# Optimization experiments

Hardware: AMD Instinct MI355X
Metric: run time of the kernel (lower is better)

Reference implementation:

```python
import jax, jax.numpy as jnp
import numpy as np

ALPHA = 1.0

def setup_inputs() -> dict:
    key = jax.random.key(0)
    k1, k2 = jax.random.split(key)
    N, D, K = 131072, 256, 256
    inputs = jax.random.normal(k1, (N, D), dtype=jnp.float32)
    clusters = jax.random.normal(k2, (K, D), dtype=jnp.float32)
    return {"inputs": inputs, "clusters": clusters}


def reference(inputs, clusters):
    x_sq = jnp.sum(inputs * inputs, axis=1, keepdims=True)          # (N,1)
    c_sq = jnp.sum(clusters * clusters, axis=1)[None, :]            # (1,K)
    cross = jnp.einsum('nd,kd->nk', inputs, clusters)               # (N,K)
    dist2 = jnp.maximum(x_sq + c_sq - 2.0 * cross, 0.0)
    q = 1.0 / (1.0 + dist2 / ALPHA)
    q = q ** ((ALPHA + 1.0) / 2.0)
    q = q / jnp.sum(q, axis=1, keepdims=True)
    return q
```

## Files before the change

kernel.cpp:

```cpp
#include <hip/hip_runtime.h>
#include <hip/hip_bf16.h>


#define DDIM 256
#define KCL 256
#define BM 128
#define DCHUNK 64

typedef __bf16 v8bf __attribute__((ext_vector_type(8)));
typedef float f32x4 __attribute__((ext_vector_type(4)));

__global__ __launch_bounds__(512, 4) void cluster_soft_assign(
    const float* __restrict__ X, const float* __restrict__ C,
    float* __restrict__ out)
{
    __shared__ __align__(16) __bf16 Bs[KCL * DCHUNK];
    __shared__ float csq_s[KCL];

    const int t    = threadIdx.x;
    const int wave = t >> 6;
    const int lane = t & 63;
    const int lr   = lane & 15;
    const int kg   = lane >> 4;

    const long brow = (long)blockIdx.x * BM;
    const int  rowl = wave * 16 + lr;
    const float* xrow = X + (brow + rowl) * DDIM;

    const int scol = t >> 1;
    const int sd0  = (t & 1) * 32;

    f32x4 acc[16];
#pragma unroll
    for (int i = 0; i < 16; ++i) { acc[i][0]=0.f; acc[i][1]=0.f; acc[i][2]=0.f; acc[i][3]=0.f; }

    float csq_part = 0.f;
    float xsq_part = 0.f;

    for (int c = 0; c < 4; ++c) {
        const int dbase = c * DCHUNK;

        const float4 a0 = *(const float4*)(xrow + dbase + kg * 8);
        const float4 a1 = *(const float4*)(xrow + dbase + kg * 8 + 4);
        const float4 a2 = *(const float4*)(xrow + dbase + 32 + kg * 8);
        const float4 a3 = *(const float4*)(xrow + dbase + 32 + kg * 8 + 4);

        if (c) __syncthreads();

        const float* cp = C + (size_t)scol * DDIM + dbase + sd0;
#pragma unroll
        for (int g = 0; g < 4; ++g) {
            const float4 f0 = *(const float4*)(cp + g * 8);
            const float4 f1 = *(const float4*)(cp + g * 8 + 4);
            csq_part += f0.x*f0.x + f0.y*f0.y + f0.z*f0.z + f0.w*f0.w
                      + f1.x*f1.x + f1.y*f1.y + f1.z*f1.z + f1.w*f1.w;
            v8bf pk;
            pk[0]=(__bf16)f0.x; pk[1]=(__bf16)f0.y; pk[2]=(__bf16)f0.z; pk[3]=(__bf16)f0.w;
            pk[4]=(__bf16)f1.x; pk[5]=(__bf16)f1.y; pk[6]=(__bf16)f1.z; pk[7]=(__bf16)f1.w;
            const int dl = sd0 + g * 8;
            *(v8bf*)&Bs[scol * DCHUNK + (dl ^ ((scol & 7) << 3))] = pk;
        }
        __syncthreads();

        xsq_part += a0.x*a0.x + a0.y*a0.y + a0.z*a0.z + a0.w*a0.w
                  + a1.x*a1.x + a1.y*a1.y + a1.z*a1.z + a1.w*a1.w
                  + a2.x*a2.x + a2.y*a2.y + a2.z*a2.z + a2.w*a2.w
                  + a3.x*a3.x + a3.y*a3.y + a3.z*a3.z + a3.w*a3.w;

        v8bf af0, af1;
        af0[0]=(__bf16)a0.x; af0[1]=(__bf16)a0.y; af0[2]=(__bf16)a0.z; af0[3]=(__bf16)a0.w;
        af0[4]=(__bf16)a1.x; af0[5]=(__bf16)a1.y; af0[6]=(__bf16)a1.z; af0[7]=(__bf16)a1.w;
        af1[0]=(__bf16)a2.x; af1[1]=(__bf16)a2.y; af1[2]=(__bf16)a2.z; af1[3]=(__bf16)a2.w;
        af1[4]=(__bf16)a3.x; af1[5]=(__bf16)a3.y; af1[6]=(__bf16)a3.z; af1[7]=(__bf16)a3.w;

        const int dl0 = kg * 8;
        const int dl1 = 32 + kg * 8;
#pragma unroll
        for (int tl = 0; tl < 16; ++tl) {
            const int col = tl * 16 + lr;
            const v8bf bf0 = *(const v8bf*)&Bs[col * DCHUNK + (dl0 ^ ((col & 7) << 3))];
            acc[tl] = __builtin_amdgcn_mfma_f32_16x16x32_bf16(af0, bf0, acc[tl], 0, 0, 0);
        }
#pragma unroll
        for (int tl = 0; tl < 16; ++tl) {
            const int col = tl * 16 + lr;
            const v8bf bf1 = *(const v8bf*)&Bs[col * DCHUNK + (dl1 ^ ((col & 7) << 3))];
            acc[tl] = __builtin_amdgcn_mfma_f32_16x16x32_bf16(af1, bf1, acc[tl], 0, 0, 0);
        }
    }

    csq_part += __shfl_xor(csq_part, 1);
    if ((t & 1) == 0) csq_s[scol] = csq_part;

    float xsq = xsq_part;
    xsq += __shfl_xor(xsq, 16);
    xsq += __shfl_xor(xsq, 32);

    __syncthreads();

#pragma unroll
    for (int j = 0; j < 4; ++j) {
        const long orow = brow + wave * 16 + kg * 4 + j;
        const float xs = __shfl(xsq, kg * 4 + j);
        float qv[16];
        float s = 0.f;
#pragma unroll
        for (int tl = 0; tl < 16; ++tl) {
            const float cs = csq_s[tl * 16 + lr];
            float d2 = xs + cs - 2.f * acc[tl][j];
            d2 = fmaxf(d2, 0.f);
            const float q = 1.f / (1.f + d2);
            qv[tl] = q;
            s += q;
        }
        s += __shfl_xor(s, 1);
        s += __shfl_xor(s, 2);
        s += __shfl_xor(s, 4);
        s += __shfl_xor(s, 8);
        const float r = 1.f / s;
        float* op = out + orow * DDIM + lr;
#pragma unroll
        for (int tl = 0; tl < 16; ++tl) op[tl * 16] = qv[tl] * r;
    }
}

extern "C" void kernel_launch(void* const* d_in, const int* in_sizes, int n_in,
                              void* d_out, int out_size, void* d_ws, size_t ws_size,
                              hipStream_t stream) {
    const float* X = (const float*)d_in[0];
    const float* C = (const float*)d_in[1];
    float* out = (float*)d_out;
    const int N = in_sizes[0] / DDIM;
    const int nblocks = N / BM;
    hipLaunchKernelGGL(cluster_soft_assign, dim3(nblocks), dim3(512), 0, stream,
                       X, C, out);
}
```

Baseline: 277.8 us.

## Make blocks persistent with full cluster matrix resident in LDS

Converts the kernel to a persistent design: 256 blocks of 1024 threads each convert and store the whole 256x256 bf16 cluster matrix in LDS once, then loop over several 256-row tiles. This removes the per-block reconversion of C and the per-chunk barriers, and adds a one-step register prefetch of X rows in the MFMA loop. The trade-off is 128KB of LDS per block, which allows only one block per CU. With 16 waves per block and a serial MFMA/epilogue per iteration, latency hiding may suffer, and the iters computation assumes N divides evenly.

```diff
diff --git a/kernel.cpp b/kernel.cpp
--- a/kernel.cpp
+++ b/kernel.cpp
@@ -4,17 +4,16 @@
 
 #define DDIM 256
 #define KCL 256
-#define BM 128
-#define DCHUNK 64
 
 typedef __bf16 v8bf __attribute__((ext_vector_type(8)));
 typedef float f32x4 __attribute__((ext_vector_type(4)));
 
-__global__ __launch_bounds__(512, 4) void cluster_soft_assign(
+__global__ __launch_bounds__(1024, 4) void cluster_soft_assign(
     const float* __restrict__ X, const float* __restrict__ C,
-    float* __restrict__ out)
+    float* __restrict__ out, int iters)
 {
-    __shared__ __align__(16) __bf16 Bs[KCL * DCHUNK];
+    __shared__ __align__(16) __bf16 Bs[KCL * DDIM];
+    __shared__ float red[1024];
     __shared__ float csq_s[KCL];
 
     const int t    = threadIdx.x;
@@ -23,33 +22,14 @@
     const int lr   = lane & 15;
     const int kg   = lane >> 4;
 
-    const long brow = (long)blockIdx.x * BM;
-    const int  rowl = wave * 16 + lr;
-    const float* xrow = X + (brow + rowl) * DDIM;
-
-    const int scol = t >> 1;
-    const int sd0  = (t & 1) * 32;
-
-    f32x4 acc[16];
+    {
+        const int col = t & 255;
+        const int dq  = (t >> 8) * 64;
+        const int sw  = (col & 7) << 3;
+        const float* cp = C + (size_t)col * DDIM + dq;
+        float csq_part = 0.f;
 #pragma unroll
-    for (int i = 0; i < 16; ++i) { acc[i][0]=0.f; acc[i][1]=0.f; acc[i][2]=0.f; acc[i][3]=0.f; }
-
-    float csq_part = 0.f;
-    float xsq_part = 0.f;
-
-    for (int c = 0; c < 4; ++c) {
-        const int dbase = c * DCHUNK;
-
-        const float4 a0 = *(const float4*)(xrow + dbase + kg * 8);
-        const float4 a1 = *(const float4*)(xrow + dbase + kg * 8 + 4);
-        const float4 a2 = *(const float4*)(xrow + dbase + 32 + kg * 8);
-        const float4 a3 = *(const float4*)(xrow + dbase + 32 + kg * 8 + 4);
-
-        if (c) __syncthreads();
-
-        const float* cp = C + (size_t)scol * DDIM + dbase + sd0;
-#pragma unroll
-        for (int g = 0; g < 4; ++g) {
+        for (int g = 0; g < 8; ++g) {
             const float4 f0 = *(const float4*)(cp + g * 8);
             const float4 f1 = *(const float4*)(cp + g * 8 + 4);
             csq_part += f0.x*f0.x + f0.y*f0.y + f0.z*f0.z + f0.w*f0.w
@@ -57,70 +37,78 @@
             v8bf pk;
             pk[0]=(__bf16)f0.x; pk[1]=(__bf16)f0.y; pk[2]=(__bf16)f0.z; pk[3]=(__bf16)f0.w;
             pk[4]=(__bf16)f1.x; pk[5]=(__bf16)f1.y; pk[6]=(__bf16)f1.z; pk[7]=(__bf16)f1.w;
-            const int dl = sd0 + g * 8;
-            *(v8bf*)&Bs[scol * DCHUNK + (dl ^ ((scol & 7) << 3))] = pk;
+            const int d = dq + g * 8;
+            *(v8bf*)&Bs[col * DDIM + (d ^ sw)] = pk;
         }
-        __syncthreads();
-
-        xsq_part += a0.x*a0.x + a0.y*a0.y + a0.z*a0.z + a0.w*a0.w
-                  + a1.x*a1.x + a1.y*a1.y + a1.z*a1.z + a1.w*a1.w
-                  + a2.x*a2.x + a2.y*a2.y + a2.z*a2.z + a2.w*a2.w
-                  + a3.x*a3.x + a3.y*a3.y + a3.z*a3.z + a3.w*a3.w;
-
-        v8bf af0, af1;
-        af0[0]=(__bf16)a0.x; af0[1]=(__bf16)a0.y; af0[2]=(__bf16)a0.z; af0[3]=(__bf16)a0.w;
-        af0[4]=(__bf16)a1.x; af0[5]=(__bf16)a1.y; af0[6]=(__bf16)a1.z; af0[7]=(__bf16)a1.w;
-        af1[0]=(__bf16)a2.x; af1[1]=(__bf16)a2.y; af1[2]=(__bf16)a2.z; af1[3]=(__bf16)a2.w;
-        af1[4]=(__bf16)a3.x; af1[5]=(__bf16)a3.y; af1[6]=(__bf16)a3.z; af1[7]=(__bf16)a3.w;
-
-        const int dl0 = kg * 8;
-        const int dl1 = 32 + kg * 8;
-#pragma unroll
-        for (int tl = 0; tl < 16; ++tl) {
-            const int col = tl * 16 + lr;
-            const v8bf bf0 = *(const v8bf*)&Bs[col * DCHUNK + (dl0 ^ ((col & 7) << 3))];
-            acc[tl] = __builtin_amdgcn_mfma_f32_16x16x32_bf16(af0, bf0, acc[tl], 0, 0, 0);
-        }
-#pragma unroll
-        for (int tl = 0; tl < 16; ++tl) {
-            const int col = tl * 16 + lr;
-            const v8bf bf1 = *(const v8bf*)&Bs[col * DCHUNK + (dl1 ^ ((col & 7) << 3))];
-            acc[tl] = __builtin_amdgcn_mfma_f32_16x16x32_bf16(af1, bf1, acc[tl], 0, 0, 0);
-        }
+        red[t] = csq_part;
     }
-
-    csq_part += __shfl_xor(csq_part, 1);
-    if ((t & 1) == 0) csq_s[scol] = csq_part;
-
-    float xsq = xsq_part;
-    xsq += __shfl_xor(xsq, 16);
-    xsq += __shfl_xor(xsq, 32);
-
+    __syncthreads();
+    if (t < 256) csq_s[t] = red[t] + red[t + 256] + red[t + 512] + red[t + 768];
     __syncthreads();
 
+    const int swl = (lr & 7) << 3;
+
+    for (int it = 0; it < iters; ++it) {
+        const size_t rowbase = ((size_t)blockIdx.x * iters + it) * 256;
+        const float* xrow = X + (rowbase + wave * 16 + lr) * DDIM + kg * 8;
+
+        f32x4 acc[16];
 #pragma unroll
-    for (int j = 0; j < 4; ++j) {
-        const long orow = brow + wave * 16 + kg * 4 + j;
-        const float xs = __shfl(xsq, kg * 4 + j);
-        float qv[16];
-        float s = 0.f;
+        for (int i = 0; i < 16; ++i) { acc[i][0]=0.f; acc[i][1]=0.f; acc[i][2]=0.f; acc[i][3]=0.f; }
+        float xsq = 0.f;
+
+        float4 c0 = *(const float4*)(xrow + 0);
+        float4 c1 = *(const float4*)(xrow + 4);
 #pragma unroll
-        for (int tl = 0; tl < 16; ++tl) {
-            const float cs = csq_s[tl * 16 + lr];
-            float d2 = xs + cs - 2.f * acc[tl][j];
-            d2 = fmaxf(d2, 0.f);
-            const float q = 1.f / (1.f + d2);
-            qv[tl] = q;
-            s += q;
+        for (int kc = 0; kc < 8; ++kc) {
+            float4 n0, n1;
+            if (kc < 7) {
+                n0 = *(const float4*)(xrow + (kc + 1) * 32);
+                n1 = *(const float4*)(xrow + (kc + 1) * 32 + 4);
+            }
+            xsq += c0.x*c0.x + c0.y*c0.y + c0.z*c0.z + c0.w*c0.w
+                 + c1.x*c1.x + c1.y*c1.y + c1.z*c1.z + c1.w*c1.w;
+            v8bf af;
+            af[0]=(__bf16)c0.x; af[1]=(__bf16)c0.y; af[2]=(__bf16)c0.z; af[3]=(__bf16)c0.w;
+            af[4]=(__bf16)c1.x; af[5]=(__bf16)c1.y; af[6]=(__bf16)c1.z; af[7]=(__bf16)c1.w;
+
+            const int dbase = kc * 32 + kg * 8;
+#pragma unroll
+            for (int tl = 0; tl < 16; ++tl) {
+                const int col = tl * 16 + lr;
+                const v8bf bf = *(const v8bf*)&Bs[col * DDIM + (dbase ^ swl)];
+                acc[tl] = __builtin_amdgcn_mfma_f32_16x16x32_bf16(af, bf, acc[tl], 0, 0, 0);
+            }
+            c0 = n0; c1 = n1;
         }
-        s += __shfl_xor(s, 1);
-        s += __shfl_xor(s, 2);
-        s += __shfl_xor(s, 4);
-        s += __shfl_xor(s, 8);
-        const float r = 1.f / s;
-        float* op = out + orow * DDIM + lr;
+
+        xsq += __shfl_xor(xsq, 16);
+        xsq += __shfl_xor(xsq, 32);
+
 #pragma unroll
-        for (int tl = 0; tl < 16; ++tl) op[tl * 16] = qv[tl] * r;
+        for (int j = 0; j < 4; ++j) {
+            const size_t orow = rowbase + wave * 16 + kg * 4 + j;
+            const float xs = __shfl(xsq, kg * 4 + j);
+            float qv[16];
+            float s = 0.f;
+#pragma unroll
+            for (int tl = 0; tl < 16; ++tl) {
+                const float cs = csq_s[tl * 16 + lr];
+                float d2 = xs + cs - 2.f * acc[tl][j];
+                d2 = fmaxf(d2, 0.f);
+                const float q = 1.f / (1.f + d2);
+                qv[tl] = q;
+                s += q;
+            }
+            s += __shfl_xor(s, 1);
+            s += __shfl_xor(s, 2);
+            s += __shfl_xor(s, 4);
+            s += __shfl_xor(s, 8);
+            const float r = 1.f / s;
+            float* op = out + orow * DDIM + lr;
+#pragma unroll
+            for (int tl = 0; tl < 16; ++tl) op[tl * 16] = qv[tl] * r;
+        }
     }
 }
 
@@ -131,7 +119,9 @@
     const float* C = (const float*)d_in[1];
     float* out = (float*)d_out;
     const int N = in_sizes[0] / DDIM;
-    const int nblocks = N / BM;
-    hipLaunchKernelGGL(cluster_soft_assign, dim3(nblocks), dim3(512), 0, stream,
-                       X, C, out);
+    int nblocks = N / 256;
+    if (nblocks > 256) nblocks = 256;
+    const int iters = N / (nblocks * 256);
+    hipLaunchKernelGGL(cluster_soft_assign, dim3(nblocks), dim3(1024), 0, stream,
+                       X, C, out, iters);
 }
```

Result: slower. 600.0 us (+116.0%).

## Double-buffer cluster tiles, prefetch X rows, and stage output through LDS for vector stores

Applied to the files above, without the earlier changes.

The cluster chunk tiles in LDS are now double-buffered, and the next chunk's global load overlaps the MFMA work on the current chunk. All X row data is loaded up front. In the epilogue, c_sq values are hoisted into registers and the divisions use hardware rcp. Output goes through an LDS transpose so each row is written with float4 coalesced stores. The costs are higher register and LDS use, a lower occupancy hint (2 instead of 4), and the reduced precision of rcp.

```diff
diff --git a/kernel.cpp b/kernel.cpp
--- a/kernel.cpp
+++ b/kernel.cpp
@@ -10,11 +10,11 @@
 typedef __bf16 v8bf __attribute__((ext_vector_type(8)));
 typedef float f32x4 __attribute__((ext_vector_type(4)));
 
-__global__ __launch_bounds__(512, 4) void cluster_soft_assign(
+__global__ __launch_bounds__(512, 2) void cluster_soft_assign(
     const float* __restrict__ X, const float* __restrict__ C,
     float* __restrict__ out)
 {
-    __shared__ __align__(16) __bf16 Bs[KCL * DCHUNK];
+    __shared__ __align__(16) __bf16 Bs[2][KCL * DCHUNK];
     __shared__ float csq_s[KCL];
 
     const int t    = threadIdx.x;
@@ -23,93 +23,117 @@
     const int lr   = lane & 15;
     const int kg   = lane >> 4;
 
-    const long brow = (long)blockIdx.x * BM;
-    const int  rowl = wave * 16 + lr;
-    const float* xrow = X + (brow + rowl) * DDIM;
+    const size_t brow = (size_t)blockIdx.x * BM;
+    const float* xrow = X + (brow + wave * 16 + lr) * DDIM + kg * 8;
 
     const int scol = t >> 1;
     const int sd0  = (t & 1) * 32;
+    const float* cbase = C + (size_t)scol * DDIM + sd0;
 
-    f32x4 acc[16];
-#pragma unroll
-    for (int i = 0; i < 16; ++i) { acc[i][0]=0.f; acc[i][1]=0.f; acc[i][2]=0.f; acc[i][3]=0.f; }
+    float4 sr[8];
+    float  csq_part = 0.f;
 
-    float csq_part = 0.f;
-    float xsq_part = 0.f;
-
-    for (int c = 0; c < 4; ++c) {
-        const int dbase = c * DCHUNK;
-
-        const float4 a0 = *(const float4*)(xrow + dbase + kg * 8);
-        const float4 a1 = *(const float4*)(xrow + dbase + kg * 8 + 4);
-        const float4 a2 = *(const float4*)(xrow + dbase + 32 + kg * 8);
-        const float4 a3 = *(const float4*)(xrow + dbase + 32 + kg * 8 + 4);
-
-        if (c) __syncthreads();
-
-        const float* cp = C + (size_t)scol * DDIM + dbase + sd0;
+    auto stage_load = [&](int c) {
+        const float* cp = cbase + c * DCHUNK;
 #pragma unroll
         for (int g = 0; g < 4; ++g) {
-            const float4 f0 = *(const float4*)(cp + g * 8);
-            const float4 f1 = *(const float4*)(cp + g * 8 + 4);
+            sr[2*g]   = *(const float4*)(cp + g * 8);
+            sr[2*g+1] = *(const float4*)(cp + g * 8 + 4);
+        }
+    };
+    auto stage_write = [&](int b) {
+#pragma unroll
+        for (int g = 0; g < 4; ++g) {
+            const float4 f0 = sr[2*g], f1 = sr[2*g+1];
             csq_part += f0.x*f0.x + f0.y*f0.y + f0.z*f0.z + f0.w*f0.w
                       + f1.x*f1.x + f1.y*f1.y + f1.z*f1.z + f1.w*f1.w;
             v8bf pk;
             pk[0]=(__bf16)f0.x; pk[1]=(__bf16)f0.y; pk[2]=(__bf16)f0.z; pk[3]=(__bf16)f0.w;
             pk[4]=(__bf16)f1.x; pk[5]=(__bf16)f1.y; pk[6]=(__bf16)f1.z; pk[7]=(__bf16)f1.w;
             const int dl = sd0 + g * 8;
-            *(v8bf*)&Bs[scol * DCHUNK + (dl ^ ((scol & 7) << 3))] = pk;
+            *(v8bf*)&Bs[b][scol * DCHUNK + (dl ^ ((scol & 7) << 3))] = pk;
         }
-        __syncthreads();
+    };
 
-        xsq_part += a0.x*a0.x + a0.y*a0.y + a0.z*a0.z + a0.w*a0.w
-                  + a1.x*a1.x + a1.y*a1.y + a1.z*a1.z + a1.w*a1.w
-                  + a2.x*a2.x + a2.y*a2.y + a2.z*a2.z + a2.w*a2.w
-                  + a3.x*a3.x + a3.y*a3.y + a3.z*a3.z + a3.w*a3.w;
+    float4 ax[16];
+#pragma unroll
+    for (int c = 0; c < 4; ++c) {
+        ax[4*c+0] = *(const float4*)(xrow + c*64);
+        ax[4*c+1] = *(const float4*)(xrow + c*64 + 4);
+        ax[4*c+2] = *(const float4*)(xrow + c*64 + 32);
+        ax[4*c+3] = *(const float4*)(xrow + c*64 + 36);
+    }
+    stage_load(0);
 
-        v8bf af0, af1;
-        af0[0]=(__bf16)a0.x; af0[1]=(__bf16)a0.y; af0[2]=(__bf16)a0.z; af0[3]=(__bf16)a0.w;
-        af0[4]=(__bf16)a1.x; af0[5]=(__bf16)a1.y; af0[6]=(__bf16)a1.z; af0[7]=(__bf16)a1.w;
-        af1[0]=(__bf16)a2.x; af1[1]=(__bf16)a2.y; af1[2]=(__bf16)a2.z; af1[3]=(__bf16)a2.w;
-        af1[4]=(__bf16)a3.x; af1[5]=(__bf16)a3.y; af1[6]=(__bf16)a3.z; af1[7]=(__bf16)a3.w;
+    float xsq = 0.f;
+    v8bf af[8];
+#pragma unroll
+    for (int c = 0; c < 4; ++c) {
+        const float4 a0 = ax[4*c], a1 = ax[4*c+1], a2 = ax[4*c+2], a3 = ax[4*c+3];
+        xsq += a0.x*a0.x + a0.y*a0.y + a0.z*a0.z + a0.w*a0.w
+             + a1.x*a1.x + a1.y*a1.y + a1.z*a1.z + a1.w*a1.w
+             + a2.x*a2.x + a2.y*a2.y + a2.z*a2.z + a2.w*a2.w
+             + a3.x*a3.x + a3.y*a3.y + a3.z*a3.z + a3.w*a3.w;
+        v8bf f0, f1;
+        f0[0]=(__bf16)a0.x; f0[1]=(__bf16)a0.y; f0[2]=(__bf16)a0.z; f0[3]=(__bf16)a0.w;
+        f0[4]=(__bf16)a1.x; f0[5]=(__bf16)a1.y; f0[6]=(__bf16)a1.z; f0[7]=(__bf16)a1.w;
+        f1[0]=(__bf16)a2.x; f1[1]=(__bf16)a2.y; f1[2]=(__bf16)a2.z; f1[3]=(__bf16)a2.w;
+        f1[4]=(__bf16)a3.x; f1[5]=(__bf16)a3.y; f1[6]=(__bf16)a3.z; f1[7]=(__bf16)a3.w;
+        af[2*c] = f0; af[2*c+1] = f1;
+    }
+    xsq += __shfl_xor(xsq, 16);
+    xsq += __shfl_xor(xsq, 32);
 
-        const int dl0 = kg * 8;
-        const int dl1 = 32 + kg * 8;
+    stage_write(0);
+    stage_load(1);
+    __syncthreads();
+
+    f32x4 acc[16];
+#pragma unroll
+    for (int i = 0; i < 16; ++i) { acc[i][0]=0.f; acc[i][1]=0.f; acc[i][2]=0.f; acc[i][3]=0.f; }
+
+#pragma unroll
+    for (int c = 0; c < 4; ++c) {
+        const int b = c & 1;
 #pragma unroll
         for (int tl = 0; tl < 16; ++tl) {
             const int col = tl * 16 + lr;
-            const v8bf bf0 = *(const v8bf*)&Bs[col * DCHUNK + (dl0 ^ ((col & 7) << 3))];
-            acc[tl] = __builtin_amdgcn_mfma_f32_16x16x32_bf16(af0, bf0, acc[tl], 0, 0, 0);
+            const v8bf bf = *(const v8bf*)&Bs[b][col * DCHUNK + ((kg*8) ^ ((col & 7) << 3))];
+            acc[tl] = __builtin_amdgcn_mfma_f32_16x16x32_bf16(af[2*c], bf, acc[tl], 0, 0, 0);
         }
 #pragma unroll
         for (int tl = 0; tl < 16; ++tl) {
             const int col = tl * 16 + lr;
-            const v8bf bf1 = *(const v8bf*)&Bs[col * DCHUNK + (dl1 ^ ((col & 7) << 3))];
-            acc[tl] = __builtin_amdgcn_mfma_f32_16x16x32_bf16(af1, bf1, acc[tl], 0, 0, 0);
+            const v8bf bf = *(const v8bf*)&Bs[b][col * DCHUNK + ((32 + kg*8) ^ ((col & 7) << 3))];
+            acc[tl] = __builtin_amdgcn_mfma_f32_16x16x32_bf16(af[2*c+1], bf, acc[tl], 0, 0, 0);
+        }
+        if (c < 3) {
+            __syncthreads();
+            stage_write(b ^ 1);
+            if (c < 2) stage_load(c + 2);
+            __syncthreads();
         }
     }
 
     csq_part += __shfl_xor(csq_part, 1);
     if ((t & 1) == 0) csq_s[scol] = csq_part;
-
-    float xsq = xsq_part;
-    xsq += __shfl_xor(xsq, 16);
-    xsq += __shfl_xor(xsq, 32);
-
     __syncthreads();
 
+    float cs[16];
+#pragma unroll
+    for (int tl = 0; tl < 16; ++tl) cs[tl] = csq_s[tl * 16 + lr];
+
+    float* tb = (float*)&Bs[0][0];
+    const int twbase = wave * 1024;
 #pragma unroll
     for (int j = 0; j < 4; ++j) {
-        const long orow = brow + wave * 16 + kg * 4 + j;
         const float xs = __shfl(xsq, kg * 4 + j);
         float qv[16];
         float s = 0.f;
 #pragma unroll
         for (int tl = 0; tl < 16; ++tl) {
-            const float cs = csq_s[tl * 16 + lr];
-            float d2 = xs + cs - 2.f * acc[tl][j];
-            d2 = fmaxf(d2, 0.f);
-            const float q = 1.f / (1.f + d2);
+            const float d2 = fmaxf(xs + cs[tl] - 2.f * acc[tl][j], 0.f);
+            const float q = __builtin_amdgcn_rcpf(1.f + d2);
             qv[tl] = q;
             s += q;
         }
@@ -117,10 +141,18 @@
         s += __shfl_xor(s, 2);
         s += __shfl_xor(s, 4);
         s += __shfl_xor(s, 8);
-        const float r = 1.f / s;
-        float* op = out + orow * DDIM + lr;
+        const float r = __builtin_amdgcn_rcpf(s);
 #pragma unroll
-        for (int tl = 0; tl < 16; ++tl) op[tl * 16] = qv[tl] * r;
+        for (int tl = 0; tl < 16; ++tl) {
+            const int col = tl * 16 + lr;
+            tb[twbase + kg * 256 + (col ^ (kg * 8))] = qv[tl] * r;
+        }
+        asm volatile("s_waitcnt lgkmcnt(0)" ::: "memory");
+#pragma unroll
+        for (int i = 0; i < 4; ++i) {
+            const f32x4 rv = *(const f32x4*)&tb[twbase + i * 256 + ((lane * 4) ^ (i * 8))];
+            *(f32x4*)&out[(brow + wave * 16 + i * 4 + j) * DDIM + lane * 4] = rv;
+        }
     }
 }
 
```

Result: faster. 271.9 us (-2.1%).

## Precompute bf16 swizzled clusters once and stream them into LDS with global_load_lds

Applied to the files above, without the earlier changes.

A small prep kernel converts the cluster matrix to bf16 in the swizzled LDS layout and computes the cluster squared norms once into workspace. The main kernel then copies each 64-wide chunk straight into LDS with global_load_lds instead of every block reloading fp32 clusters, converting them and re-reducing the norms. The main kernel also halves the rows per block with 256 threads and prefetches the next X chunk before the MFMAs. It uses hardware rcp approximations and stages each output row through LDS so stores are full-row coalesced float4 writes. The trade-offs are an extra launch and slightly less precise reciprocals.

```diff
diff --git a/kernel.cpp b/kernel.cpp
--- a/kernel.cpp
+++ b/kernel.cpp
@@ -3,16 +3,42 @@
 
 
 #define DDIM 256
-#define KCL 256
-#define BM 128
+#define KCL  256
+#define BM   64
 #define DCHUNK 64
 
 typedef __bf16 v8bf __attribute__((ext_vector_type(8)));
+typedef __bf16 v4bf __attribute__((ext_vector_type(4)));
 typedef float f32x4 __attribute__((ext_vector_type(4)));
 
-__global__ __launch_bounds__(512, 4) void cluster_soft_assign(
-    const float* __restrict__ X, const float* __restrict__ C,
-    float* __restrict__ out)
+__global__ __launch_bounds__(256) void prep_clusters(
+    const float* __restrict__ C, __bf16* __restrict__ wsB, float* __restrict__ wsCsq)
+{
+    const int t = threadIdx.x;
+    const int wave = t >> 6, lane = t & 63;
+    const int col = blockIdx.x * 4 + wave;
+    const float4 v = *(const float4*)(C + (size_t)col * DDIM + lane * 4);
+    float cs = v.x*v.x + v.y*v.y + v.z*v.z + v.w*v.w;
+    cs += __shfl_xor(cs, 1);  cs += __shfl_xor(cs, 2);  cs += __shfl_xor(cs, 4);
+    cs += __shfl_xor(cs, 8);  cs += __shfl_xor(cs, 16); cs += __shfl_xor(cs, 32);
+    if (lane == 0) wsCsq[col] = cs;
+    const int chunk = lane >> 4;
+    const int dcb   = (lane * 4) & 63;
+    const int sw    = (col & 7) << 3;
+    v4bf pk;
+    pk[0] = (__bf16)v.x; pk[1] = (__bf16)v.y; pk[2] = (__bf16)v.z; pk[3] = (__bf16)v.w;
+    *(v4bf*)&wsB[chunk * 16384 + col * DCHUNK + (dcb ^ sw)] = pk;
+}
+
+__device__ __forceinline__ void gload_lds16(const void* g, void* l) {
+    __builtin_amdgcn_global_load_lds(
+        (const __attribute__((address_space(1))) unsigned int*)g,
+        (__attribute__((address_space(3))) unsigned int*)l, 16, 0, 0);
+}
+
+__global__ __launch_bounds__(256, 4) void cluster_soft_assign(
+    const float* __restrict__ X, const __bf16* __restrict__ wsB,
+    const float* __restrict__ wsCsq, float* __restrict__ out)
 {
     __shared__ __align__(16) __bf16 Bs[KCL * DCHUNK];
     __shared__ float csq_s[KCL];
@@ -23,93 +49,85 @@
     const int lr   = lane & 15;
     const int kg   = lane >> 4;
 
-    const long brow = (long)blockIdx.x * BM;
-    const int  rowl = wave * 16 + lr;
-    const float* xrow = X + (brow + rowl) * DDIM;
+    const size_t brow = (size_t)blockIdx.x * BM;
+    const float* xrow = X + (brow + wave * 16 + lr) * DDIM + kg * 8;
 
-    const int scol = t >> 1;
-    const int sd0  = (t & 1) * 32;
+    csq_s[t] = wsCsq[t];
+
+    float4 ax0 = *(const float4*)(xrow + 0);
+    float4 ax1 = *(const float4*)(xrow + 4);
+    float4 ax2 = *(const float4*)(xrow + 32);
+    float4 ax3 = *(const float4*)(xrow + 36);
 
     f32x4 acc[16];
 #pragma unroll
     for (int i = 0; i < 16; ++i) { acc[i][0]=0.f; acc[i][1]=0.f; acc[i][2]=0.f; acc[i][3]=0.f; }
-
-    float csq_part = 0.f;
-    float xsq_part = 0.f;
+    float xsq = 0.f;
+    const int swl = (lr & 7) << 3;
 
     for (int c = 0; c < 4; ++c) {
-        const int dbase = c * DCHUNK;
-
-        const float4 a0 = *(const float4*)(xrow + dbase + kg * 8);
-        const float4 a1 = *(const float4*)(xrow + dbase + kg * 8 + 4);
-        const float4 a2 = *(const float4*)(xrow + dbase + 32 + kg * 8);
-        const float4 a3 = *(const float4*)(xrow + dbase + 32 + kg * 8 + 4);
-
-        if (c) __syncthreads();
-
-        const float* cp = C + (size_t)scol * DDIM + dbase + sd0;
-#pragma unroll
-        for (int g = 0; g < 4; ++g) {
-            const float4 f0 = *(const float4*)(cp + g * 8);
-            const float4 f1 = *(const float4*)(cp + g * 8 + 4);
-            csq_part += f0.x*f0.x + f0.y*f0.y + f0.z*f0.z + f0.w*f0.w
-                      + f1.x*f1.x + f1.y*f1.y + f1.z*f1.z + f1.w*f1.w;
-            v8bf pk;
-            pk[0]=(__bf16)f0.x; pk[1]=(__bf16)f0.y; pk[2]=(__bf16)f0.z; pk[3]=(__bf16)f0.w;
-            pk[4]=(__bf16)f1.x; pk[5]=(__bf16)f1.y; pk[6]=(__bf16)f1.z; pk[7]=(__bf16)f1.w;
-            const int dl = sd0 + g * 8;
-            *(v8bf*)&Bs[scol * DCHUNK + (dl ^ ((scol & 7) << 3))] = pk;
-        }
         __syncthreads();
 
-        xsq_part += a0.x*a0.x + a0.y*a0.y + a0.z*a0.z + a0.w*a0.w
-                  + a1.x*a1.x + a1.y*a1.y + a1.z*a1.z + a1.w*a1.w
-                  + a2.x*a2.x + a2.y*a2.y + a2.z*a2.z + a2.w*a2.w
-                  + a3.x*a3.x + a3.y*a3.y + a3.z*a3.z + a3.w*a3.w;
+        const __bf16* src = wsB + c * 16384;
+#pragma unroll
+        for (int i = 0; i < 8; ++i) {
+            const int seg = wave * 8 + i;
+            gload_lds16(src + seg * 512 + lane * 8, &Bs[seg * 512]);
+        }
 
         v8bf af0, af1;
-        af0[0]=(__bf16)a0.x; af0[1]=(__bf16)a0.y; af0[2]=(__bf16)a0.z; af0[3]=(__bf16)a0.w;
-        af0[4]=(__bf16)a1.x; af0[5]=(__bf16)a1.y; af0[6]=(__bf16)a1.z; af0[7]=(__bf16)a1.w;
-        af1[0]=(__bf16)a2.x; af1[1]=(__bf16)a2.y; af1[2]=(__bf16)a2.z; af1[3]=(__bf16)a2.w;
-        af1[4]=(__bf16)a3.x; af1[5]=(__bf16)a3.y; af1[6]=(__bf16)a3.z; af1[7]=(__bf16)a3.w;
+        af0[0]=(__bf16)ax0.x; af0[1]=(__bf16)ax0.y; af0[2]=(__bf16)ax0.z; af0[3]=(__bf16)ax0.w;
+        af0[4]=(__bf16)ax1.x; af0[5]=(__bf16)ax1.y; af0[6]=(__bf16)ax1.z; af0[7]=(__bf16)ax1.w;
+        af1[0]=(__bf16)ax2.x; af1[1]=(__bf16)ax2.y; af1[2]=(__bf16)ax2.z; af1[3]=(__bf16)ax2.w;
+        af1[4]=(__bf16)ax3.x; af1[5]=(__bf16)ax3.y; af1[6]=(__bf16)ax3.z; af1[7]=(__bf16)ax3.w;
+        xsq += ax0.x*ax0.x + ax0.y*ax0.y + ax0.z*ax0.z + ax0.w*ax0.w
+             + ax1.x*ax1.x + ax1.y*ax1.y + ax1.z*ax1.z + ax1.w*ax1.w
+             + ax2.x*ax2.x + ax2.y*ax2.y + ax2.z*ax2.z + ax2.w*ax2.w
+             + ax3.x*ax3.x + ax3.y*ax3.y + ax3.z*ax3.z + ax3.w*ax3.w;
 
-        const int dl0 = kg * 8;
-        const int dl1 = 32 + kg * 8;
+        __syncthreads();
+
+        if (c < 3) {
+            const float* xp = xrow + (c + 1) * 64;
+            ax0 = *(const float4*)(xp);
+            ax1 = *(const float4*)(xp + 4);
+            ax2 = *(const float4*)(xp + 32);
+            ax3 = *(const float4*)(xp + 36);
+        }
+
 #pragma unroll
         for (int tl = 0; tl < 16; ++tl) {
             const int col = tl * 16 + lr;
-            const v8bf bf0 = *(const v8bf*)&Bs[col * DCHUNK + (dl0 ^ ((col & 7) << 3))];
-            acc[tl] = __builtin_amdgcn_mfma_f32_16x16x32_bf16(af0, bf0, acc[tl], 0, 0, 0);
+            const v8bf b0 = *(const v8bf*)&Bs[col * DCHUNK + ((kg * 8) ^ swl)];
+            acc[tl] = __builtin_amdgcn_mfma_f32_16x16x32_bf16(af0, b0, acc[tl], 0, 0, 0);
         }
 #pragma unroll
         for (int tl = 0; tl < 16; ++tl) {
             const int col = tl * 16 + lr;
-            const v8bf bf1 = *(const v8bf*)&Bs[col * DCHUNK + (dl1 ^ ((col & 7) << 3))];
-            acc[tl] = __builtin_amdgcn_mfma_f32_16x16x32_bf16(af1, bf1, acc[tl], 0, 0, 0);
+            const v8bf b1 = *(const v8bf*)&Bs[col * DCHUNK + ((32 + kg * 8) ^ swl)];
+            acc[tl] = __builtin_amdgcn_mfma_f32_16x16x32_bf16(af1, b1, acc[tl], 0, 0, 0);
         }
     }
 
-    csq_part += __shfl_xor(csq_part, 1);
-    if ((t & 1) == 0) csq_s[scol] = csq_part;
-
-    float xsq = xsq_part;
     xsq += __shfl_xor(xsq, 16);
     xsq += __shfl_xor(xsq, 32);
 
+    float cs_[16];
+#pragma unroll
+    for (int tl = 0; tl < 16; ++tl) cs_[tl] = csq_s[tl * 16 + lr];
+
     __syncthreads();
 
+    float* tb = (float*)&Bs[0] + wave * 1024;
 #pragma unroll
     for (int j = 0; j < 4; ++j) {
-        const long orow = brow + wave * 16 + kg * 4 + j;
         const float xs = __shfl(xsq, kg * 4 + j);
         float qv[16];
         float s = 0.f;
 #pragma unroll
         for (int tl = 0; tl < 16; ++tl) {
-            const float cs = csq_s[tl * 16 + lr];
-            float d2 = xs + cs - 2.f * acc[tl][j];
-            d2 = fmaxf(d2, 0.f);
-            const float q = 1.f / (1.f + d2);
+            const float d2 = fmaxf(xs + cs_[tl] - 2.f * acc[tl][j], 0.f);
+            const float q = __builtin_amdgcn_rcpf(1.f + d2);
             qv[tl] = q;
             s += q;
         }
@@ -117,10 +135,18 @@
         s += __shfl_xor(s, 2);
         s += __shfl_xor(s, 4);
         s += __shfl_xor(s, 8);
-        const float r = 1.f / s;
-        float* op = out + orow * DDIM + lr;
+        const float r = __builtin_amdgcn_rcpf(s);
 #pragma unroll
-        for (int tl = 0; tl < 16; ++tl) op[tl * 16] = qv[tl] * r;
+        for (int tl = 0; tl < 16; ++tl) {
+            const int col = tl * 16 + lr;
+            tb[kg * 256 + (col ^ (kg * 8))] = qv[tl] * r;
+        }
+        asm volatile("s_waitcnt lgkmcnt(0)" ::: "memory");
+#pragma unroll
+        for (int i = 0; i < 4; ++i) {
+            const f32x4 rv = *(const f32x4*)&tb[i * 256 + ((lane * 4) ^ (i * 8))];
+            *(f32x4*)&out[(brow + wave * 16 + i * 4 + j) * DDIM + lane * 4] = rv;
+        }
     }
 }
 
@@ -130,8 +156,12 @@
     const float* X = (const float*)d_in[0];
     const float* C = (const float*)d_in[1];
     float* out = (float*)d_out;
+    __bf16* wsB   = (__bf16*)d_ws;
+    float*  wsCsq = (float*)((char*)d_ws + KCL * DDIM * 2);
     const int N = in_sizes[0] / DDIM;
     const int nblocks = N / BM;
-    hipLaunchKernelGGL(cluster_soft_assign, dim3(nblocks), dim3(512), 0, stream,
-                       X, C, out);
+
+    hipLaunchKernelGGL(prep_clusters, dim3(KCL / 4), dim3(256), 0, stream, C, wsB, wsCsq);
+    hipLaunchKernelGGL(cluster_soft_assign, dim3(nblocks), dim3(256), 0, stream,
+                       X, wsB, wsCsq, out);
 }
```

Result: faster. 247.7 us (-10.9%).
